# Performance work log

Hardware: AMD Instinct MI355X
Metric: run time of the kernel (lower is better)

Reference implementation:

```python
import jax, jax.numpy as jnp
import numpy as np

N = 100000
C = 32            # channels per degree (shape_in == shape_out == 32)
NI = C * C        # flattened Gram-matrix size = n_input = n_hidden
LN_EPS = 1e-5
SLOPE = 0.01      # LeakyReLU default negative slope


def _ln(x, g, b):
    mu = jnp.mean(x, axis=-1, keepdims=True)
    var = jnp.var(x, axis=-1, keepdims=True)  # biased, matches torch LayerNorm
    return (x - mu) * jax.lax.rsqrt(var + LN_EPS) * g + b


def _lrelu(x):
    return jnp.where(x >= 0, x, SLOPE * x)


def _gal(v, g1, b1, w1, g2, b2, w2, bias2):
    # v: [N, ch_in, m]
    n, ci, _ = v.shape
    dot = jnp.einsum('nac,nbc->nab', v, v).reshape(n, ci * ci)  # Gram matrix
    dot = jnp.sign(dot) * jnp.maximum(jnp.abs(dot), 1e-12)
    h = _lrelu(_ln(dot, g1, b1)) @ w1.T           # [N, ch_in*ch_out]
    h = _lrelu(_ln(h, g2, b2)) @ w2.T + bias2      # [N, ch_in*ch_out]
    attn = jax.nn.softmax(h.reshape(n, -1, ci), axis=-1)  # [N, ch_out, ch_in]
    return jnp.einsum('nab,nbc->nac', attn, v)     # [N, ch_out, m]


def _mk_type_params(key):
    ks = jax.random.split(key, 3)
    bound = np.sqrt(6.0 / NI)  # kaiming_uniform_, fan_in=NI
    return dict(
        ln1_g=jnp.ones((NI,), jnp.float32),
        ln1_b=jnp.zeros((NI,), jnp.float32),
        w1=jax.random.uniform(ks[0], (NI, NI), jnp.float32, -bound, bound),
        ln2_g=jnp.ones((NI,), jnp.float32),
        ln2_b=jnp.zeros((NI,), jnp.float32),
        w2=jax.random.uniform(ks[1], (NI, NI), jnp.float32, -bound, bound),
        b2=jax.random.uniform(ks[2], (NI,), jnp.float32, -1.0 / C, 1.0 / C),
    )


def setup_inputs():
    key = jax.random.key(0)
    k0, k1, kp0, kp1 = jax.random.split(key, 4)
    d = {
        'f0': jax.random.normal(k0, (N, C, 1), jnp.float32),
        'f1': jax.random.normal(k1, (N, C, 3), jnp.float32),
    }
    for tag, kk in (('0', kp0), ('1', kp1)):
        p = _mk_type_params(kk)
        for name, val in p.items():
            d[f'{name}_{tag}'] = val
    return d


def reference(f0, f1,
              ln1_g_0, ln1_b_0, w1_0, ln2_g_0, ln2_b_0, w2_0, b2_0,
              ln1_g_1, ln1_b_1, w1_1, ln2_g_1, ln2_b_1, w2_1, b2_1):
    out0 = _gal(f0, ln1_g_0, ln1_b_0, w1_0, ln2_g_0, ln2_b_0, w2_0, b2_0)
    out1 = _gal(f1, ln1_g_1, ln1_b_1, w1_1, ln2_g_1, ln2_b_1, w2_1, b2_1)
    return (out0, out1)
```

## Files before the change

### kernel.cpp

```cpp
#include <hip/hip_runtime.h>

#define NN     100000
#define NB     1563
#define LN_EPS 1e-5f
#define SLOPE  0.01f

typedef __bf16 bf16x8 __attribute__((ext_vector_type(8)));
typedef float  f32x4  __attribute__((ext_vector_type(4)));
typedef unsigned short u16;
typedef unsigned int   u32;

union Pack8 { uint4 u4; bf16x8 bf; u16 s[8]; };

__device__ __forceinline__ u16 f2bf(float x){
    u32 b = __float_as_uint(x);
    b += 0x7fffu + ((b >> 16) & 1u);
    return (u16)(b >> 16);
}

__global__ __launch_bounds__(1024) void prep_weights(
    const float* __restrict__ wa, const float* __restrict__ wb,
    const float* __restrict__ wc, const float* __restrict__ wd,
    u16* __restrict__ dst)
{
    int m = blockIdx.y;
    const float* src = (m==0)? wa : (m==1)? wb : (m==2)? wc : wd;
    u16* d = dst + (size_t)m * (1024u*1024u);
    int tid = blockIdx.x * blockDim.x + threadIdx.x;
    int sub = tid & 3;
    int row = (tid >> 2) & 1023;
    int kb  = tid >> 12;
    const float4* s4 = (const float4*)(src + row*1024 + kb*32 + sub*8);
    float4 a = s4[0], b = s4[1];
    Pack8 p;
    p.s[0]=f2bf(a.x); p.s[1]=f2bf(a.y); p.s[2]=f2bf(a.z); p.s[3]=f2bf(a.w);
    p.s[4]=f2bf(b.x); p.s[5]=f2bf(b.y); p.s[6]=f2bf(b.z); p.s[7]=f2bf(b.w);
    ((uint4*)d)[(kb*1024 + row)*4 + sub] = p.u4;
}

__device__ __forceinline__ void gemm_quad(
    const u16* __restrict__ Wp, const u16* xs,
    int wv, int lane15, int q, f32x4 acc[4][4])
{
    const uint4* bA = (const uint4*)Wp + (wv*32 + lane15)*4 + q;
    const uint4* bB = (const uint4*)Wp + ((wv+16)*32 + lane15)*4 + q;
    const uint4* ab = (const uint4*)xs + q*64 + lane15;
    #pragma unroll
    for (int ct=0; ct<4; ++ct)
      #pragma unroll
      for (int rt=0; rt<4; ++rt)
        acc[ct][rt] = (f32x4){0.f,0.f,0.f,0.f};
    uint4 nb0 = bA[0], nb1 = bA[64], nb2 = bB[0], nb3 = bB[64];
    #pragma unroll 4
    for (int ks=0; ks<32; ++ks){
        Pack8 b0, b1, b2, b3, a0, a1, a2, a3;
        b0.u4 = nb0; b1.u4 = nb1; b2.u4 = nb2; b3.u4 = nb3;
        const int kn = (ks+1) & 31;
        nb0 = bA[kn*4096];
        nb1 = bA[kn*4096 + 64];
        nb2 = bB[kn*4096];
        nb3 = bB[kn*4096 + 64];
        a0.u4 = ab[ks*256];
        a1.u4 = ab[ks*256 + 16];
        a2.u4 = ab[ks*256 + 32];
        a3.u4 = ab[ks*256 + 48];
        acc[0][0] = __builtin_amdgcn_mfma_f32_16x16x32_bf16(a0.bf, b0.bf, acc[0][0], 0,0,0);
        acc[0][1] = __builtin_amdgcn_mfma_f32_16x16x32_bf16(a1.bf, b0.bf, acc[0][1], 0,0,0);
        acc[0][2] = __builtin_amdgcn_mfma_f32_16x16x32_bf16(a2.bf, b0.bf, acc[0][2], 0,0,0);
        acc[0][3] = __builtin_amdgcn_mfma_f32_16x16x32_bf16(a3.bf, b0.bf, acc[0][3], 0,0,0);
        acc[1][0] = __builtin_amdgcn_mfma_f32_16x16x32_bf16(a0.bf, b1.bf, acc[1][0], 0,0,0);
        acc[1][1] = __builtin_amdgcn_mfma_f32_16x16x32_bf16(a1.bf, b1.bf, acc[1][1], 0,0,0);
        acc[1][2] = __builtin_amdgcn_mfma_f32_16x16x32_bf16(a2.bf, b1.bf, acc[1][2], 0,0,0);
        acc[1][3] = __builtin_amdgcn_mfma_f32_16x16x32_bf16(a3.bf, b1.bf, acc[1][3], 0,0,0);
        acc[2][0] = __builtin_amdgcn_mfma_f32_16x16x32_bf16(a0.bf, b2.bf, acc[2][0], 0,0,0);
        acc[2][1] = __builtin_amdgcn_mfma_f32_16x16x32_bf16(a1.bf, b2.bf, acc[2][1], 0,0,0);
        acc[2][2] = __builtin_amdgcn_mfma_f32_16x16x32_bf16(a2.bf, b2.bf, acc[2][2], 0,0,0);
        acc[2][3] = __builtin_amdgcn_mfma_f32_16x16x32_bf16(a3.bf, b2.bf, acc[2][3], 0,0,0);
        acc[3][0] = __builtin_amdgcn_mfma_f32_16x16x32_bf16(a0.bf, b3.bf, acc[3][0], 0,0,0);
        acc[3][1] = __builtin_amdgcn_mfma_f32_16x16x32_bf16(a1.bf, b3.bf, acc[3][1], 0,0,0);
        acc[3][2] = __builtin_amdgcn_mfma_f32_16x16x32_bf16(a2.bf, b3.bf, acc[3][2], 0,0,0);
        acc[3][3] = __builtin_amdgcn_mfma_f32_16x16x32_bf16(a3.bf, b3.bf, acc[3][3], 0,0,0);
    }
}

template<int MDIM>
__global__ __launch_bounds__(1024, 4) void gal_fused(
    const float* __restrict__ f,
    const float* __restrict__ ln1g, const float* __restrict__ ln1b,
    const float* __restrict__ ln2g, const float* __restrict__ ln2b,
    const float* __restrict__ b2,
    const u16* __restrict__ Wp1, const u16* __restrict__ Wp2,
    float* __restrict__ outp)
{
    extern __shared__ char smem[];
    constexpr int VSTR = 32*MDIM + 4;
    constexpr int SBS  = 64*32 + 4;
    u16*   xs    = (u16*)smem;
    float* sbuf  = (float*)smem;
    float* vbuf  = (float*)smem + 32832;
    float* stats = (float*)smem + 32832 + 64*VSTR;

    const int tid    = threadIdx.x;
    const int lane   = tid & 63;
    const int wv     = tid >> 6;
    const int lane15 = lane & 15;
    const int q      = lane >> 4;
    const int node0  = blockIdx.x * 64;

    if (tid < 128) stats[tid] = 0.f;
    {
        float4* vbuf4 = (float4*)vbuf;
        const int gv4  = node0*8*MDIM;
        const int lim4 = NN*8*MDIM;
        for (int i = tid; i < 64*8*MDIM; i += 1024){
            int nd = i / (8*MDIM);
            int r4 = i - nd*(8*MDIM);
            float4 val = (gv4 + i < lim4) ? ((const float4*)f)[gv4 + i]
                                          : (float4){0.f,0.f,0.f,0.f};
            vbuf4[nd*(VSTR/4) + r4] = val;
        }
    }
    __syncthreads();

    {
        const int n = tid >> 4;
        const int j = tid & 15;
        const float* vn = vbuf + n*VSTR;
        float va[2][MDIM];
        #pragma unroll
        for (int c=0;c<MDIM;++c){ va[0][c]=vn[(j*2)*MDIM+c]; va[1][c]=vn[(j*2+1)*MDIM+c]; }
        float sum=0.f, ssum=0.f;
        #pragma unroll
        for (int b=0;b<32;++b){
            float d0=0.f, d1=0.f;
            #pragma unroll
            for (int c=0;c<MDIM;++c){ float vb = vn[b*MDIM+c]; d0 += va[0][c]*vb; d1 += va[1][c]*vb; }
            sum += d0+d1; ssum += d0*d0 + d1*d1;
        }
        #pragma unroll
        for (int st=1; st<16; st<<=1){ sum += __shfl_xor(sum, st); ssum += __shfl_xor(ssum, st); }
        float mu   = sum * (1.f/1024.f);
        float rstd = rsqrtf(ssum*(1.f/1024.f) - mu*mu + LN_EPS);
        #pragma unroll
        for (int jb=0;jb<8;++jb){
            const int k0 = j*64 + jb*8;
            float4 ga = ((const float4*)(ln1g + k0))[0];
            float4 gb = ((const float4*)(ln1g + k0))[1];
            float4 ba = ((const float4*)(ln1b + k0))[0];
            float4 bb = ((const float4*)(ln1b + k0))[1];
            float gg[8] = {ga.x,ga.y,ga.z,ga.w,gb.x,gb.y,gb.z,gb.w};
            float bbv[8] = {ba.x,ba.y,ba.z,ba.w,bb.x,bb.y,bb.z,bb.w};
            Pack8 p;
            const int ai = jb >> 2;
            #pragma unroll
            for (int l=0;l<8;++l){
                int b = (jb*8+l) & 31;
                float d = 0.f;
                #pragma unroll
                for (int c=0;c<MDIM;++c) d += va[ai][c]*vn[b*MDIM+c];
                float x = (d - mu)*rstd*gg[l] + bbv[l];
                x = (x >= 0.f)? x : SLOPE*x;
                p.s[l] = f2bf(x);
            }
            ((uint4*)xs)[(j*8+jb)*64 + n] = p.u4;
        }
    }
    __syncthreads();

    {
        f32x4 acc[4][4];
        gemm_quad(Wp1, xs, wv, lane15, q, acc);
        {
            float p_[16], pp_[16];
            #pragma unroll
            for (int idx=0; idx<16; ++idx){
                int rt = idx>>2, rr = idx&3;
                float s=0.f, s2=0.f;
                #pragma unroll
                for (int ct=0; ct<4; ++ct){
                    float h = acc[ct][rt][rr];
                    s += h; s2 += h*h;
                }
                p_[idx] = s; pp_[idx] = s2;
            }
            #pragma unroll
            for (int m=8; m>=1; m>>=1){
                const bool hi = (lane15 & m) != 0;
                #pragma unroll
                for (int i=0; i<m; ++i){
                    float sp = hi ? p_[i]  : p_[i+m];
                    float kp = hi ? p_[i+m]  : p_[i];
                    p_[i]  = kp + __shfl_xor(sp, m);
                    float sq = hi ? pp_[i] : pp_[i+m];
                    float kq = hi ? pp_[i+m] : pp_[i];
                    pp_[i] = kq + __shfl_xor(sq, m);
                }
            }
            int nd = (lane15>>2)*16 + q*4 + (lane15&3);
            atomicAdd(&stats[2*nd],   p_[0]);
            atomicAdd(&stats[2*nd+1], pp_[0]);
        }
        __syncthreads();

        float g2c[4], b2c[4];
        #pragma unroll
        for (int ct=0; ct<4; ++ct){
            int col = (wv + (ct>>1)*16)*32 + (ct&1)*16 + lane15;
            g2c[ct] = ln2g[col];
            b2c[ct] = ln2b[col];
        }
        #pragma unroll
        for (int rt=0; rt<4; ++rt)
          #pragma unroll
          for (int rr=0; rr<4; ++rr){
            int nd = rt*16 + q*4 + rr;
            float mu   = stats[2*nd]*(1.f/1024.f);
            float rstd = rsqrtf(stats[2*nd+1]*(1.f/1024.f) - mu*mu + LN_EPS);
            #pragma unroll
            for (int ct=0; ct<4; ++ct){
                float h = acc[ct][rt][rr];
                float x = (h - mu)*rstd*g2c[ct] + b2c[ct];
                x = (x >= 0.f)? x : SLOPE*x;
                int col = (wv + (ct>>1)*16)*32 + (ct&1)*16 + lane15;
                xs[(col>>3)*512 + nd*8 + (col&7)] = f2bf(x);
            }
          }
    }
    __syncthreads();

    {
        f32x4 acc[4][4];
        gemm_quad(Wp2, xs, wv, lane15, q, acc);
        float bias[4];
        #pragma unroll
        for (int ct=0; ct<4; ++ct)
            bias[ct] = b2[(wv + (ct>>1)*16)*32 + (ct&1)*16 + lane15];
        __syncthreads();

        #pragma unroll
        for (int si=0; si<2; ++si){
            #pragma unroll
            for (int ctl=0; ctl<2; ++ctl){
                const int ct = si*2 + ctl;
                #pragma unroll
                for (int rt=0; rt<4; ++rt)
                  #pragma unroll
                  for (int rr=0; rr<4; ++rr){
                    int nd = rt*16 + q*4 + rr;
                    sbuf[wv*SBS + nd*32 + ctl*16 + lane15] = acc[ct][rt][rr] + bias[ct];
                  }
            }
            __syncthreads();
            {
                const int nd  = tid >> 4;
                const int a15 = tid & 15;
                const float* hp = sbuf + a15*SBS + nd*32;
                float e[32];
                #pragma unroll
                for (int r=0;r<8;++r){
                    float4 v4 = ((const float4*)hp)[r];
                    e[4*r]=v4.x; e[4*r+1]=v4.y; e[4*r+2]=v4.z; e[4*r+3]=v4.w;
                }
                float mx = e[0];
                #pragma unroll
                for (int b=1;b<32;++b) mx = fmaxf(mx, e[b]);
                float sm = 0.f;
                #pragma unroll
                for (int b=0;b<32;++b){ e[b] = __expf(e[b]-mx); sm += e[b]; }
                float inv = 1.f / sm;
                float oacc[MDIM];
                #pragma unroll
                for (int c=0;c<MDIM;++c) oacc[c]=0.f;
                const float4* vr = (const float4*)(vbuf + nd*VSTR);
                #pragma unroll
                for (int r=0; r<8*MDIM; ++r){
                    float4 v4 = vr[r];
                    #pragma unroll
                    for (int t=0;t<4;++t){
                        const int fi = 4*r+t;
                        const int b  = fi/MDIM;
                        const int c  = fi - b*MDIM;
                        float comp = (t==0)?v4.x:(t==1)?v4.y:(t==2)?v4.z:v4.w;
                        oacc[c] += e[b]*comp;
                    }
                }
                int ng = node0 + nd;
                if (ng < NN){
                    #pragma unroll
                    for (int c=0;c<MDIM;++c)
                        outp[((size_t)ng*32 + a15 + si*16)*MDIM + c] = oacc[c]*inv;
                }
            }
            if (si==0) __syncthreads();
        }
    }
}

extern "C" void kernel_launch(void* const* d_in, const int* in_sizes, int n_in,
                              void* d_out, int out_size, void* d_ws, size_t ws_size,
                              hipStream_t stream)
{
    const float* f0    = (const float*)d_in[0];
    const float* f1    = (const float*)d_in[1];
    const float* ln1g0 = (const float*)d_in[2];
    const float* ln1b0 = (const float*)d_in[3];
    const float* w1_0  = (const float*)d_in[4];
    const float* ln2g0 = (const float*)d_in[5];
    const float* ln2b0 = (const float*)d_in[6];
    const float* w2_0  = (const float*)d_in[7];
    const float* b2_0  = (const float*)d_in[8];
    const float* ln1g1 = (const float*)d_in[9];
    const float* ln1b1 = (const float*)d_in[10];
    const float* w1_1  = (const float*)d_in[11];
    const float* ln2g1 = (const float*)d_in[12];
    const float* ln2b1 = (const float*)d_in[13];
    const float* w2_1  = (const float*)d_in[14];
    const float* b2_1  = (const float*)d_in[15];
    float* out = (float*)d_out;
    u16* wp = (u16*)d_ws;

    const int smem1 = (32832 + 64*(32*1+4) + 128)*4;
    const int smem3 = (32832 + 64*(32*3+4) + 128)*4;
    (void)hipFuncSetAttribute(reinterpret_cast<const void*>(&gal_fused<1>),
                              hipFuncAttributeMaxDynamicSharedMemorySize, smem1);
    (void)hipFuncSetAttribute(reinterpret_cast<const void*>(&gal_fused<3>),
                              hipFuncAttributeMaxDynamicSharedMemorySize, smem3);

    prep_weights<<<dim3(128,4), 1024, 0, stream>>>(w1_0, w2_0, w1_1, w2_1, wp);
    gal_fused<1><<<NB, 1024, smem1, stream>>>(f0, ln1g0, ln1b0, ln2g0, ln2b0, b2_0,
                                              wp,            wp + 1048576, out);
    gal_fused<3><<<NB, 1024, smem3, stream>>>(f1, ln1g1, ln1b1, ln2g1, ln2b1, b2_1,
                                              wp + 2097152,  wp + 3145728, out + (size_t)NN*32);
}
```

Measured before the change: 1.512 ms.

## Halve block to 8 waves, each computing a 128-column GEMM tile

Changes the fused kernel from 1024 to 512 threads per block. Each wave now owns 128 contiguous output columns (8 MFMA column tiles × 4 row tiles) instead of 64 split columns, so every LDS activation fragment is reused across twice as many weight tiles. The LayerNorm-1, LN2 and softmax/output stages are re-indexed to the new thread-to-work mapping, with four softmax passes instead of two. The explicit software prefetch of weight fragments is dropped in favour of loading all 8 B fragments per k-step. In exchange, accumulator register pressure doubles and each CU runs half as many waves, which reduces latency hiding.

```diff
diff --git a/kernel.cpp b/kernel.cpp
--- a/kernel.cpp
+++ b/kernel.cpp
@@ -38,53 +38,34 @@
     ((uint4*)d)[(kb*1024 + row)*4 + sub] = p.u4;
 }
 
-__device__ __forceinline__ void gemm_quad(
+__device__ __forceinline__ void gemm_oct(
     const u16* __restrict__ Wp, const u16* xs,
-    int wv, int lane15, int q, f32x4 acc[4][4])
+    int wv, int lane15, int q, f32x4 acc[8][4])
 {
-    const uint4* bA = (const uint4*)Wp + (wv*32 + lane15)*4 + q;
-    const uint4* bB = (const uint4*)Wp + ((wv+16)*32 + lane15)*4 + q;
-    const uint4* ab = (const uint4*)xs + q*64 + lane15;
+    const uint4* Wp4 = (const uint4*)Wp + (wv*128 + lane15)*4 + q;
+    const uint4* ab  = (const uint4*)xs + q*64 + lane15;
     #pragma unroll
-    for (int ct=0; ct<4; ++ct)
+    for (int t=0; t<8; ++t)
       #pragma unroll
       for (int rt=0; rt<4; ++rt)
-        acc[ct][rt] = (f32x4){0.f,0.f,0.f,0.f};
-    uint4 nb0 = bA[0], nb1 = bA[64], nb2 = bB[0], nb3 = bB[64];
-    #pragma unroll 4
+        acc[t][rt] = (f32x4){0.f,0.f,0.f,0.f};
+    #pragma unroll 2
     for (int ks=0; ks<32; ++ks){
-        Pack8 b0, b1, b2, b3, a0, a1, a2, a3;
-        b0.u4 = nb0; b1.u4 = nb1; b2.u4 = nb2; b3.u4 = nb3;
-        const int kn = (ks+1) & 31;
-        nb0 = bA[kn*4096];
-        nb1 = bA[kn*4096 + 64];
-        nb2 = bB[kn*4096];
-        nb3 = bB[kn*4096 + 64];
-        a0.u4 = ab[ks*256];
-        a1.u4 = ab[ks*256 + 16];
-        a2.u4 = ab[ks*256 + 32];
-        a3.u4 = ab[ks*256 + 48];
-        acc[0][0] = __builtin_amdgcn_mfma_f32_16x16x32_bf16(a0.bf, b0.bf, acc[0][0], 0,0,0);
-        acc[0][1] = __builtin_amdgcn_mfma_f32_16x16x32_bf16(a1.bf, b0.bf, acc[0][1], 0,0,0);
-        acc[0][2] = __builtin_amdgcn_mfma_f32_16x16x32_bf16(a2.bf, b0.bf, acc[0][2], 0,0,0);
-        acc[0][3] = __builtin_amdgcn_mfma_f32_16x16x32_bf16(a3.bf, b0.bf, acc[0][3], 0,0,0);
-        acc[1][0] = __builtin_amdgcn_mfma_f32_16x16x32_bf16(a0.bf, b1.bf, acc[1][0], 0,0,0);
-        acc[1][1] = __builtin_amdgcn_mfma_f32_16x16x32_bf16(a1.bf, b1.bf, acc[1][1], 0,0,0);
-        acc[1][2] = __builtin_amdgcn_mfma_f32_16x16x32_bf16(a2.bf, b1.bf, acc[1][2], 0,0,0);
-        acc[1][3] = __builtin_amdgcn_mfma_f32_16x16x32_bf16(a3.bf, b1.bf, acc[1][3], 0,0,0);
-        acc[2][0] = __builtin_amdgcn_mfma_f32_16x16x32_bf16(a0.bf, b2.bf, acc[2][0], 0,0,0);
-        acc[2][1] = __builtin_amdgcn_mfma_f32_16x16x32_bf16(a1.bf, b2.bf, acc[2][1], 0,0,0);
-        acc[2][2] = __builtin_amdgcn_mfma_f32_16x16x32_bf16(a2.bf, b2.bf, acc[2][2], 0,0,0);
-        acc[2][3] = __builtin_amdgcn_mfma_f32_16x16x32_bf16(a3.bf, b2.bf, acc[2][3], 0,0,0);
-        acc[3][0] = __builtin_amdgcn_mfma_f32_16x16x32_bf16(a0.bf, b3.bf, acc[3][0], 0,0,0);
-        acc[3][1] = __builtin_amdgcn_mfma_f32_16x16x32_bf16(a1.bf, b3.bf, acc[3][1], 0,0,0);
-        acc[3][2] = __builtin_amdgcn_mfma_f32_16x16x32_bf16(a2.bf, b3.bf, acc[3][2], 0,0,0);
-        acc[3][3] = __builtin_amdgcn_mfma_f32_16x16x32_bf16(a3.bf, b3.bf, acc[3][3], 0,0,0);
+        Pack8 b[8], a[4];
+        #pragma unroll
+        for (int t=0; t<8; ++t) b[t].u4 = Wp4[ks*4096 + t*64];
+        #pragma unroll
+        for (int rt=0; rt<4; ++rt) a[rt].u4 = ab[ks*256 + rt*16];
+        #pragma unroll
+        for (int t=0; t<8; ++t)
+          #pragma unroll
+          for (int rt=0; rt<4; ++rt)
+            acc[t][rt] = __builtin_amdgcn_mfma_f32_16x16x32_bf16(a[rt].bf, b[t].bf, acc[t][rt], 0,0,0);
     }
 }
 
 template<int MDIM>
-__global__ __launch_bounds__(1024, 4) void gal_fused(
+__global__ __launch_bounds__(512, 2) void gal_fused(
     const float* __restrict__ f,
     const float* __restrict__ ln1g, const float* __restrict__ ln1b,
     const float* __restrict__ ln2g, const float* __restrict__ ln2b,
@@ -112,7 +93,7 @@
         float4* vbuf4 = (float4*)vbuf;
         const int gv4  = node0*8*MDIM;
         const int lim4 = NN*8*MDIM;
-        for (int i = tid; i < 64*8*MDIM; i += 1024){
+        for (int i = tid; i < 64*8*MDIM; i += 512){
             int nd = i / (8*MDIM);
             int r4 = i - nd*(8*MDIM);
             float4 val = (gv4 + i < lim4) ? ((const float4*)f)[gv4 + i]
@@ -123,32 +104,40 @@
     __syncthreads();
 
     {
-        const int n = tid >> 4;
-        const int j = tid & 15;
+        const int n = tid >> 3;
+        const int j = tid & 7;
         const float* vn = vbuf + n*VSTR;
-        float va[2][MDIM];
-        #pragma unroll
-        for (int c=0;c<MDIM;++c){ va[0][c]=vn[(j*2)*MDIM+c]; va[1][c]=vn[(j*2+1)*MDIM+c]; }
+        float va[4][MDIM];
+        #pragma unroll
+        for (int i=0;i<4;++i)
+          #pragma unroll
+          for (int c=0;c<MDIM;++c) va[i][c] = vn[(j*4+i)*MDIM+c];
         float sum=0.f, ssum=0.f;
         #pragma unroll
         for (int b=0;b<32;++b){
-            float d0=0.f, d1=0.f;
-            #pragma unroll
-            for (int c=0;c<MDIM;++c){ float vb = vn[b*MDIM+c]; d0 += va[0][c]*vb; d1 += va[1][c]*vb; }
-            sum += d0+d1; ssum += d0*d0 + d1*d1;
-        }
-        #pragma unroll
-        for (int st=1; st<16; st<<=1){ sum += __shfl_xor(sum, st); ssum += __shfl_xor(ssum, st); }
+            float vb[MDIM];
+            #pragma unroll
+            for (int c=0;c<MDIM;++c) vb[c] = vn[b*MDIM+c];
+            #pragma unroll
+            for (int i=0;i<4;++i){
+                float d=0.f;
+                #pragma unroll
+                for (int c=0;c<MDIM;++c) d += va[i][c]*vb[c];
+                sum += d; ssum += d*d;
+            }
+        }
+        #pragma unroll
+        for (int st=1; st<8; st<<=1){ sum += __shfl_xor(sum, st); ssum += __shfl_xor(ssum, st); }
         float mu   = sum * (1.f/1024.f);
         float rstd = rsqrtf(ssum*(1.f/1024.f) - mu*mu + LN_EPS);
         #pragma unroll
-        for (int jb=0;jb<8;++jb){
-            const int k0 = j*64 + jb*8;
+        for (int jb=0;jb<16;++jb){
+            const int k0 = j*128 + jb*8;
             float4 ga = ((const float4*)(ln1g + k0))[0];
             float4 gb = ((const float4*)(ln1g + k0))[1];
             float4 ba = ((const float4*)(ln1b + k0))[0];
             float4 bb = ((const float4*)(ln1b + k0))[1];
-            float gg[8] = {ga.x,ga.y,ga.z,ga.w,gb.x,gb.y,gb.z,gb.w};
+            float gg[8]  = {ga.x,ga.y,ga.z,ga.w,gb.x,gb.y,gb.z,gb.w};
             float bbv[8] = {ba.x,ba.y,ba.z,ba.w,bb.x,bb.y,bb.z,bb.w};
             Pack8 p;
             const int ai = jb >> 2;
@@ -162,14 +151,14 @@
                 x = (x >= 0.f)? x : SLOPE*x;
                 p.s[l] = f2bf(x);
             }
-            ((uint4*)xs)[(j*8+jb)*64 + n] = p.u4;
+            ((uint4*)xs)[(j*16+jb)*64 + n] = p.u4;
         }
     }
     __syncthreads();
 
     {
-        f32x4 acc[4][4];
-        gemm_quad(Wp1, xs, wv, lane15, q, acc);
+        f32x4 acc[8][4];
+        gemm_oct(Wp1, xs, wv, lane15, q, acc);
         {
             float p_[16], pp_[16];
             #pragma unroll
@@ -177,8 +166,8 @@
                 int rt = idx>>2, rr = idx&3;
                 float s=0.f, s2=0.f;
                 #pragma unroll
-                for (int ct=0; ct<4; ++ct){
-                    float h = acc[ct][rt][rr];
+                for (int t=0; t<8; ++t){
+                    float h = acc[t][rt][rr];
                     s += h; s2 += h*h;
                 }
                 p_[idx] = s; pp_[idx] = s2;
@@ -202,12 +191,12 @@
         }
         __syncthreads();
 
-        float g2c[4], b2c[4];
-        #pragma unroll
-        for (int ct=0; ct<4; ++ct){
-            int col = (wv + (ct>>1)*16)*32 + (ct&1)*16 + lane15;
-            g2c[ct] = ln2g[col];
-            b2c[ct] = ln2b[col];
+        float g2c[8], b2c[8];
+        #pragma unroll
+        for (int t=0; t<8; ++t){
+            int col = wv*128 + t*16 + lane15;
+            g2c[t] = ln2g[col];
+            b2c[t] = ln2b[col];
         }
         #pragma unroll
         for (int rt=0; rt<4; ++rt)
@@ -217,11 +206,11 @@
             float mu   = stats[2*nd]*(1.f/1024.f);
             float rstd = rsqrtf(stats[2*nd+1]*(1.f/1024.f) - mu*mu + LN_EPS);
             #pragma unroll
-            for (int ct=0; ct<4; ++ct){
-                float h = acc[ct][rt][rr];
-                float x = (h - mu)*rstd*g2c[ct] + b2c[ct];
+            for (int t=0; t<8; ++t){
+                float h = acc[t][rt][rr];
+                float x = (h - mu)*rstd*g2c[t] + b2c[t];
                 x = (x >= 0.f)? x : SLOPE*x;
-                int col = (wv + (ct>>1)*16)*32 + (ct&1)*16 + lane15;
+                int col = wv*128 + t*16 + lane15;
                 xs[(col>>3)*512 + nd*8 + (col&7)] = f2bf(x);
             }
           }
@@ -229,32 +218,32 @@
     __syncthreads();
 
     {
-        f32x4 acc[4][4];
-        gemm_quad(Wp2, xs, wv, lane15, q, acc);
-        float bias[4];
-        #pragma unroll
-        for (int ct=0; ct<4; ++ct)
-            bias[ct] = b2[(wv + (ct>>1)*16)*32 + (ct&1)*16 + lane15];
+        f32x4 acc[8][4];
+        gemm_oct(Wp2, xs, wv, lane15, q, acc);
+        float bias[8];
+        #pragma unroll
+        for (int t=0; t<8; ++t)
+            bias[t] = b2[wv*128 + t*16 + lane15];
         __syncthreads();
 
         #pragma unroll
-        for (int si=0; si<2; ++si){
+        for (int si=0; si<4; ++si){
             #pragma unroll
             for (int ctl=0; ctl<2; ++ctl){
-                const int ct = si*2 + ctl;
+                const int t = si*2 + ctl;
                 #pragma unroll
                 for (int rt=0; rt<4; ++rt)
                   #pragma unroll
                   for (int rr=0; rr<4; ++rr){
                     int nd = rt*16 + q*4 + rr;
-                    sbuf[wv*SBS + nd*32 + ctl*16 + lane15] = acc[ct][rt][rr] + bias[ct];
+                    sbuf[wv*SBS + nd*32 + ctl*16 + lane15] = acc[t][rt][rr] + bias[t];
                   }
             }
             __syncthreads();
             {
-                const int nd  = tid >> 4;
-                const int a15 = tid & 15;
-                const float* hp = sbuf + a15*SBS + nd*32;
+                const int nd = tid >> 3;
+                const int w8 = tid & 7;
+                const float* hp = sbuf + w8*SBS + nd*32;
                 float e[32];
                 #pragma unroll
                 for (int r=0;r<8;++r){
@@ -286,12 +275,13 @@
                 }
                 int ng = node0 + nd;
                 if (ng < NN){
+                    const int a = w8*4 + si;
                     #pragma unroll
                     for (int c=0;c<MDIM;++c)
-                        outp[((size_t)ng*32 + a15 + si*16)*MDIM + c] = oacc[c]*inv;
-                }
-            }
-            if (si==0) __syncthreads();
+                        outp[((size_t)ng*32 + a)*MDIM + c] = oacc[c]*inv;
+                }
+            }
+            if (si<3) __syncthreads();
         }
     }
 }
@@ -327,8 +317,8 @@
                               hipFuncAttributeMaxDynamicSharedMemorySize, smem3);
 
     prep_weights<<<dim3(128,4), 1024, 0, stream>>>(w1_0, w2_0, w1_1, w2_1, wp);
-    gal_fused<1><<<NB, 1024, smem1, stream>>>(f0, ln1g0, ln1b0, ln2g0, ln2b0, b2_0,
-                                              wp,            wp + 1048576, out);
-    gal_fused<3><<<NB, 1024, smem3, stream>>>(f1, ln1g1, ln1b1, ln2g1, ln2b1, b2_1,
-                                              wp + 2097152,  wp + 3145728, out + (size_t)NN*32);
-}
+    gal_fused<1><<<NB, 512, smem1, stream>>>(f0, ln1g0, ln1b0, ln2g0, ln2b0, b2_0,
+                                             wp,            wp + 1048576, out);
+    gal_fused<3><<<NB, 512, smem3, stream>>>(f1, ln1g1, ln1b1, ln2g1, ln2b1, b2_1,
+                                             wp + 2097152,  wp + 3145728, out + (size_t)NN*32);
+}
```

After: 1.708 ms. 13.0% more time.
